# Kernel optimization log

Hardware: AMD Instinct MI355X
Metric: run time of the kernel (lower is better)

## Reference

```python
import jax, jax.numpy as jnp
import numpy as np

INPUT_SIZE = 256
NUM_LABELS = 50
L = NUM_LABELS + 1  # internal label count incl. pad label (index L-1)
B, T = 64, 256


def setup_inputs() -> dict:
    key = jax.random.key(0)
    k = jax.random.split(key, 8)
    inp = {
        "input": jax.random.normal(k[0], (B, T, INPUT_SIZE), dtype=jnp.float32),
        "mask": jnp.ones((B, T), dtype=jnp.float32),
        "target": jax.random.randint(k[1], (B, T), 0, NUM_LABELS),
        # state_nn: Linear(input_size, L)
        "state_W": jax.random.normal(k[2], (INPUT_SIZE, L), dtype=jnp.float32) * 0.05,
        "state_b": jnp.zeros((L,), dtype=jnp.float32),
        # trans_nn: Linear(input_size, L*L) (bigram=True)
        "trans_W": jax.random.normal(k[3], (INPUT_SIZE, L * L), dtype=jnp.float32) * 0.05,
        "trans_b": jnp.zeros((L * L,), dtype=jnp.float32),
    }
    return inp


def _energy(x, mask, state_W, state_b, trans_W, trans_b):
    # out_s: [B,T,L]  (unary scores), out_t: [B,T,L,L] (bigram transitions)
    out_s = jnp.einsum("bti,il->btl", x, state_W) + state_b
    out_t = (jnp.einsum("bti,io->bto", x, trans_W) + trans_b).reshape(
        x.shape[0], x.shape[1], L, L
    )
    energy = out_t + out_s[:, :, None, :]  # [B,T,L,L]
    return energy * mask[:, :, None, None]


def reference(input, mask, target, state_W, state_b, trans_W, trans_b):
    """ChainCRF.loss: -log p(target | input) per batch element, shape [B]."""
    energy = _energy(input, mask, state_W, state_b, trans_W, trans_b)
    e_t = jnp.transpose(energy, (1, 0, 2, 3))  # [T,B,L,L]
    tgt_t = target.T                            # [T,B]
    msk_t = mask.T                              # [T,B]
    bidx = jnp.arange(input.shape[0])

    # t = 0: start from pad label (index L-1)
    partition0 = e_t[0][:, L - 1, :]                       # [B,L]
    tgt0 = e_t[0][bidx, L - 1, tgt_t[0]]                   # [B]

    def step(carry, xs):
        part, tgt_e, prev = carry
        curr, tgt, m = xs  # curr [B,L,L], tgt [B], m [B]
        part_new = jax.nn.logsumexp(curr + part[:, :, None], axis=1)
        part = part + (part_new - part) * m[:, None]
        tgt_e = tgt_e + curr[bidx, prev, tgt]
        return (part, tgt_e, tgt), None

    (part, tgt_e, _), _ = jax.lax.scan(
        step, (partition0, tgt0, tgt_t[0]), (e_t[1:], tgt_t[1:], msk_t[1:])
    )
    return jax.nn.logsumexp(part, axis=1) - tgt_e
```

## Files before the change

### kernel.cpp

```cpp
#include <hip/hip_runtime.h>
#include <hip/hip_bf16.h>

#define B_    64
#define T_    256
#define K_    256
#define L_    51
#define LL_   2601
#define RS_   64
#define NG_   3328
#define PST_  4096
#define MT_   128
#define NT_   128

typedef __bf16 bf16x8 __attribute__((ext_vector_type(8)));
typedef float  f32x4  __attribute__((ext_vector_type(4)));
typedef unsigned int u32x4 __attribute__((ext_vector_type(4)));
typedef u32x4 __attribute__((may_alias)) u32x4_a;

static __device__ __forceinline__ bf16x8 as_bf16x8(u32x4 u) {
    return __builtin_bit_cast(bf16x8, u);
}
static __device__ __forceinline__ unsigned short bf16bits(float x) {
    return __builtin_bit_cast(unsigned short, __float2bfloat16(x));
}
static __device__ __forceinline__ void gld_lds16(const void* g, void* l) {
    __builtin_amdgcn_global_load_lds(
        (const __attribute__((address_space(1))) unsigned int*)g,
        (__attribute__((address_space(3))) unsigned int*)l, 16, 0, 0);
}

#define DPP_STEP(v, OP, CTRL)                                                   \
    {                                                                           \
        int _x = __builtin_bit_cast(int, v);                                    \
        float _o = __builtin_bit_cast(                                          \
            float, __builtin_amdgcn_update_dpp(_x, _x, CTRL, 0xF, 0xF, true));  \
        v = OP(v, _o);                                                          \
    }
static __device__ __forceinline__ float addf(float a, float b) { return a + b; }

__global__ __launch_bounds__(256) void prep_w(
    const float* __restrict__ trans_W, const float* __restrict__ trans_b,
    const float* __restrict__ state_W, const float* __restrict__ state_b,
    __hip_bfloat16* __restrict__ Wt, float* __restrict__ bias)
{
    const int n  = blockIdx.x * 64 + (threadIdx.x >> 2);
    const int kq = (threadIdx.x & 3) * 64;
    const int j  = n >> 6;
    const int i  = n & 63;
    const bool valid = (i < L_) && (j < L_);
    const int o = i * L_ + j;

    __hip_bfloat16 tmp[64];
#pragma unroll
    for (int kk = 0; kk < 64; ++kk) {
        const int k = kq + kk;
        float w = valid ? (trans_W[(size_t)k * LL_ + o] + state_W[k * L_ + j]) : 0.f;
        tmp[kk] = __float2bfloat16(w);
    }
    u32x4* dst = (u32x4*)(Wt + (size_t)n * K_ + kq);
    const u32x4* src = (const u32x4*)tmp;
#pragma unroll
    for (int q = 0; q < 8; ++q) dst[q] = src[q];

    if ((threadIdx.x & 3) == 0)
        bias[n] = valid ? (trans_b[o] + state_b[j]) : 0.f;
}

__global__ void prep_x(const float4* __restrict__ x4, ushort4* __restrict__ xb4, int n4)
{
    for (int idx = blockIdx.x * blockDim.x + threadIdx.x; idx < n4;
         idx += gridDim.x * blockDim.x) {
        float4 v = x4[idx];
        ushort4 o;
        o.x = bf16bits(v.x); o.y = bf16bits(v.y);
        o.z = bf16bits(v.z); o.w = bf16bits(v.w);
        xb4[idx] = o;
    }
}

__global__ void zero_pad(u32x4* __restrict__ P16, int nBT)
{
    const int per = (PST_ - NG_) / 8;
    const int tot = nBT * per;
    const u32x4 z = {};
    for (int idx = blockIdx.x * blockDim.x + threadIdx.x; idx < tot;
         idx += gridDim.x * blockDim.x) {
        const int m = idx / per;
        const int q = idx - m * per;
        P16[(size_t)m * (PST_ / 8) + (NG_ / 8) + q] = z;
    }
}

__global__ __launch_bounds__(256) void gemm_energy(
    const __hip_bfloat16* __restrict__ xb,
    const __hip_bfloat16* __restrict__ Wt,
    const float* __restrict__ bias,
    const float* __restrict__ mask,
    __hip_bfloat16* __restrict__ P,
    int t0, int Tc, int TcShift)
{
    __shared__ __align__(16) __hip_bfloat16 As[MT_ * 128];
    __shared__ __align__(16) __hip_bfloat16 Bs[NT_ * 128];

    const int tid  = threadIdx.x;
    const int lane = tid & 63;
    const int wv   = tid >> 6;
    const int quad = lane >> 4;
    const int l16  = lane & 15;
    const int m0 = blockIdx.y * MT_;
    const int n0 = blockIdx.x * NT_;
    const int mrow0 = (wv >> 1) * 64;
    const int ncol0 = (wv & 1) * 64;

    const int srow = wv * 4 + (lane >> 4);
    const int spos = lane & 15;

    f32x4 acc[4][4] = {};

    for (int kp = 0; kp < 2; ++kp) {
        if (kp) __syncthreads();
#pragma unroll
        for (int it = 0; it < 8; ++it) {
            const int r  = it * 16 + srow;
            const int kc = spos ^ (r & 15);
            const int ma = m0 + r;
            const int rg = (ma >> TcShift) * T_ + t0 + (ma & (Tc - 1));
            gld_lds16((const char*)xb + (size_t)rg * 512 + kp * 256 + kc * 16,
                      (char*)As + it * 4096 + wv * 1024);
            gld_lds16((const char*)Wt + (size_t)(n0 + r) * 512 + kp * 256 + kc * 16,
                      (char*)Bs + it * 4096 + wv * 1024);
        }
        asm volatile("s_waitcnt vmcnt(0)" ::: "memory");
        __syncthreads();

        const u32x4_a* Av = (const u32x4_a*)As;
        const u32x4_a* Bv = (const u32x4_a*)Bs;
#pragma unroll
        for (int kk = 0; kk < 4; ++kk) {
            bf16x8 af[4], bfr[4];
#pragma unroll
            for (int f = 0; f < 4; ++f) {
                const int ra = mrow0 + f * 16 + l16;
                af[f]  = as_bf16x8(Av[ra * 16 + ((kk * 4 + quad) ^ (ra & 15))]);
                const int rb = ncol0 + f * 16 + l16;
                bfr[f] = as_bf16x8(Bv[rb * 16 + ((kk * 4 + quad) ^ (rb & 15))]);
            }
#pragma unroll
            for (int mf = 0; mf < 4; ++mf)
#pragma unroll
                for (int nf = 0; nf < 4; ++nf)
                    acc[mf][nf] = __builtin_amdgcn_mfma_f32_16x16x32_bf16(
                        af[mf], bfr[nf], acc[mf][nf], 0, 0, 0);
        }
    }

    float bv[4]; bool val[4]; int ncol[4], ic[4], jc[4];
#pragma unroll
    for (int nf = 0; nf < 4; ++nf) {
        const int n = n0 + ncol0 + nf * 16 + l16;
        ncol[nf] = n;
        ic[nf] = n & 63;
        jc[nf] = n >> 6;
        val[nf] = (ic[nf] < L_) && (jc[nf] < L_);
        bv[nf]  = bias[n];
    }
#pragma unroll
    for (int mf = 0; mf < 4; ++mf) {
#pragma unroll
        for (int r = 0; r < 4; ++r) {
            const int mloc = m0 + mrow0 + mf * 16 + quad * 4 + r;
            const int bb = mloc >> TcShift;
            const int tl = mloc & (Tc - 1);
            const int t  = t0 + tl;
            const float mval = mask[bb * T_ + t];
            const bool idmask = (mval == 0.f) && (t != 0);
            __hip_bfloat16* prow = P + (size_t)mloc * PST_;
#pragma unroll
            for (int nf = 0; nf < 4; ++nf) {
                float v;
                if (idmask)
                    v = (val[nf] && ic[nf] == jc[nf]) ? 1.f : 0.f;
                else
                    v = val[nf] ? __expf((acc[mf][nf][r] + bv[nf]) * mval) : 0.f;
                prow[ncol[nf]] = __float2bfloat16(v);
            }
        }
    }
}

__global__ __launch_bounds__(256) void prod_quad(
    const __hip_bfloat16* __restrict__ P,
    __hip_bfloat16* __restrict__ Q,
    int Tc)
{
    __shared__ u32x4 Sm[3][512];
    __shared__ __align__(16) unsigned short GL[64 * 72];
    __shared__ __align__(16) unsigned short VT[2][64 * 72];

    const int tid  = threadIdx.x;
    const int wv   = tid >> 6;
    const int lane = tid & 63;
    const int quad = lane >> 4;
    const int l16  = lane & 15;
    const int bq = blockIdx.x;
    const int Tq = Tc >> 2;
    const int b  = bq / Tq;
    const int tq = bq - b * Tq;
    const __hip_bfloat16* tile0 = P + (size_t)(b * Tc + tq * 4) * PST_;

    for (int q = 0; q < 6; ++q) {
        const int idx  = q * 4 + wv;
        const int tile = idx >> 3;
        const int part = idx & 7;
        const int slot = part * 64 + lane;
        const int r    = slot >> 3;
        const int csrc = (slot & 7) ^ (r & 7);
        gld_lds16((const char*)(tile0 + (size_t)(tile + 1) * PST_) + (r * 8 + csrc) * 16,
                  (char*)&Sm[tile][part * 64]);
    }
    const u32x4* g1 = (const u32x4*)tile0;
    u32x4 c0 = g1[tid], c1 = g1[256 + tid];
    asm volatile("s_waitcnt vmcnt(0)" ::: "memory");
    {
        const unsigned short* e0 = (const unsigned short*)&c0;
        const unsigned short* e1 = (const unsigned short*)&c1;
        int j = tid >> 3, i0 = (tid & 7) * 8;
#pragma unroll
        for (int e = 0; e < 8; ++e) GL[(i0 + e) * 72 + j] = e0[e];
        j = (256 + tid) >> 3; i0 = (tid & 7) * 8;
#pragma unroll
        for (int e = 0; e < 8; ++e) GL[(i0 + e) * 72 + j] = e1[e];
    }
    __syncthreads();

    __hip_bfloat16* qout = Q + (size_t)bq * PST_;
    const int ra = wv * 16 + l16;

#pragma unroll
    for (int st = 0; st < 3; ++st) {
        const u32x4* Sa = Sm[st];
        const unsigned short* Bbuf = (st == 0) ? GL : VT[st - 1];
        bf16x8 a[2], bb[4][2];
#pragma unroll
        for (int ks = 0; ks < 2; ++ks)
            a[ks] = as_bf16x8(Sa[ra * 8 + ((ks * 4 + quad) ^ (ra & 7))]);
#pragma unroll
        for (int nf = 0; nf < 4; ++nf) {
            const u32x4_a* brow = (const u32x4_a*)(Bbuf + (nf * 16 + l16) * 72);
#pragma unroll
            for (int ks = 0; ks < 2; ++ks) bb[nf][ks] = as_bf16x8(brow[ks * 4 + quad]);
        }
        f32x4 acc[4] = {};
#pragma unroll
        for (int nf = 0; nf < 4; ++nf) {
            acc[nf] = __builtin_amdgcn_mfma_f32_16x16x32_bf16(a[0], bb[nf][0], acc[nf], 0, 0, 0);
            acc[nf] = __builtin_amdgcn_mfma_f32_16x16x32_bf16(a[1], bb[nf][1], acc[nf], 0, 0, 0);
        }
        if (st < 2) {
#pragma unroll
            for (int nf = 0; nf < 4; ++nf) {
                const int n  = nf * 16 + l16;
                const int mm = wv * 16 + quad * 4;
#pragma unroll
                for (int pr = 0; pr < 2; ++pr) {
                    unsigned int pk = (unsigned int)bf16bits(acc[nf][pr * 2]) |
                                      ((unsigned int)bf16bits(acc[nf][pr * 2 + 1]) << 16);
                    *(unsigned int*)(&VT[st][n * 72 + mm + pr * 2]) = pk;
                }
            }
            __syncthreads();
        } else {
#pragma unroll
            for (int nf = 0; nf < 4; ++nf) {
                const int n = nf * 16 + l16;
#pragma unroll
                for (int r = 0; r < 4; ++r)
                    qout[(wv * 16 + quad * 4 + r) * RS_ + n] = __float2bfloat16(acc[nf][r]);
            }
        }
    }
}

__global__ __launch_bounds__(64) void tgt_kernel(
    const __hip_bfloat16* __restrict__ P, const int* __restrict__ target,
    const float* __restrict__ mask, float* __restrict__ tgt_ws, int t0, int Tc)
{
    const int b = blockIdx.x, lane = threadIdx.x;
    float s = 0.f;
    for (int tl = lane; tl < Tc; tl += 64) {
        const int t = t0 + tl;
        const int j = target[b * T_ + t];
        const int i = (t == 0) ? (L_ - 1) : target[b * T_ + t - 1];
        const float m = (t == 0) ? 1.f : mask[b * T_ + t];
        if (m != 0.f) {
            const float pval = __bfloat162float(P[(size_t)(b * Tc + tl) * PST_ + j * RS_ + i]);
            s += __logf(pval);
        }
    }
#pragma unroll
    for (int d = 1; d < 64; d <<= 1) s += __shfl_xor(s, d);
    if (lane == 0) {
        if (t0 == 0) tgt_ws[b] = s;
        else         tgt_ws[b] += s;
    }
}

__global__ __launch_bounds__(64, 1) void scan_q(
    const __hip_bfloat16* __restrict__ Q,
    float* __restrict__ p_ws, float* __restrict__ ls_ws,
    const float* __restrict__ tgt_ws, float* __restrict__ out,
    int t0q, int Tq, int Tqtot)
{
    __shared__ __align__(16) unsigned short p_arr[64];

    const int b    = blockIdx.x;
    const int lane = threadIdx.x;
    const int quad = lane >> 4;
    const int l16  = lane & 15;

    float pv[4] = {0.f, 0.f, 0.f, 0.f};
    float logscale = 0.f;
    if (t0q == 0) {
        p_arr[lane] = (lane == L_ - 1) ? (unsigned short)0x3F80 : (unsigned short)0;
    } else {
#pragma unroll
        for (int f = 0; f < 4; ++f) pv[f] = p_ws[b * 64 + f * 16 + l16];
        logscale = ls_ws[b];
        p_arr[quad * 16 + l16] = bf16bits(pv[quad]);
    }
    asm volatile("s_waitcnt lgkmcnt(0)" ::: "memory");

    int off[8];
#pragma unroll
    for (int f = 0; f < 4; ++f)
#pragma unroll
        for (int ks = 0; ks < 2; ++ks)
            off[f * 2 + ks] = (f * 16 + l16) * 8 + ks * 4 + quad;

    const u32x4* gp = (const u32x4*)Q + (size_t)b * Tq * (PST_ / 8);
    const u32x4_a* pa = (const u32x4_a*)p_arr;

    u32x4 s0[8], s1[8], s2[8], s3[8];
    auto fetch = [&](u32x4 (&st)[8], int tl) {
        const u32x4* g = gp + (size_t)tl * (PST_ / 8);
#pragma unroll
        for (int q = 0; q < 8; ++q) st[q] = g[off[q]];
    };
    fetch(s0, 0);
    if (1 < Tq) fetch(s1, 1);
    if (2 < Tq) fetch(s2, 2);
    if (3 < Tq) fetch(s3, 3);

    auto step = [&](u32x4 (&st)[8], int tl) {
        bf16x8 a0 = as_bf16x8(pa[quad]);
        bf16x8 a1 = as_bf16x8(pa[4 + quad]);
        const f32x4 z = {};
        f32x4 ae[4], ao[4];
#pragma unroll
        for (int f = 0; f < 4; ++f) {
            ae[f] = __builtin_amdgcn_mfma_f32_16x16x32_bf16(a0, as_bf16x8(st[f * 2 + 0]), z, 0, 0, 0);
            ao[f] = __builtin_amdgcn_mfma_f32_16x16x32_bf16(a1, as_bf16x8(st[f * 2 + 1]), z, 0, 0, 0);
        }
#pragma unroll
        for (int f = 0; f < 4; ++f) pv[f] = ae[f][0] + ao[f][0];

        if (((tl & 1) == 1) || (tl == Tq - 1)) {
            float mx = fmaxf(fmaxf(pv[0], pv[1]), fmaxf(pv[2], pv[3]));
            DPP_STEP(mx, fmaxf, 0xB1);
            DPP_STEP(mx, fmaxf, 0x4E);
            DPP_STEP(mx, fmaxf, 0x124);
            DPP_STEP(mx, fmaxf, 0x128);
            const float inv = 1.f / mx;
            logscale += __logf(mx);
#pragma unroll
            for (int f = 0; f < 4; ++f) pv[f] *= inv;
        }
        p_arr[quad * 16 + l16] = bf16bits(pv[quad]);
        asm volatile("s_waitcnt lgkmcnt(0)" ::: "memory");
    };

    for (int tl = 0; tl < Tq; tl += 4) {
        step(s0, tl);
        if (tl + 4 < Tq) fetch(s0, tl + 4);
        if (tl + 1 < Tq) { step(s1, tl + 1); if (tl + 5 < Tq) fetch(s1, tl + 5); }
        if (tl + 2 < Tq) { step(s2, tl + 2); if (tl + 6 < Tq) fetch(s2, tl + 6); }
        if (tl + 3 < Tq) { step(s3, tl + 3); if (tl + 7 < Tq) fetch(s3, tl + 7); }
    }

    if (t0q + Tq == Tqtot) {
        float s = pv[0] + pv[1] + pv[2] + pv[3];
        DPP_STEP(s, addf, 0xB1);
        DPP_STEP(s, addf, 0x4E);
        DPP_STEP(s, addf, 0x124);
        DPP_STEP(s, addf, 0x128);
        if (lane == 0) out[b] = logscale + __logf(s) - tgt_ws[b];
    } else {
        if (quad == 0) {
#pragma unroll
            for (int f = 0; f < 4; ++f) p_ws[b * 64 + f * 16 + l16] = pv[f];
        }
        if (lane == 0) ls_ws[b] = logscale;
    }
}

extern "C" void kernel_launch(void* const* d_in, const int* in_sizes, int n_in,
                              void* d_out, int out_size, void* d_ws, size_t ws_size,
                              hipStream_t stream)
{
    (void)in_sizes; (void)n_in; (void)out_size;
    const float* x       = (const float*)d_in[0];
    const float* mask    = (const float*)d_in[1];
    const int*   target  = (const int*)d_in[2];
    const float* state_W = (const float*)d_in[3];
    const float* state_b = (const float*)d_in[4];
    const float* trans_W = (const float*)d_in[5];
    const float* trans_b = (const float*)d_in[6];
    float* out = (float*)d_out;

    char* ws = (char*)d_ws;
    size_t off = 0;
    auto alloc = [&](size_t bytes) -> void* {
        void* p = ws + off;
        off = (off + bytes + 255) & ~(size_t)255;
        return p;
    };

    __hip_bfloat16* Wt   = (__hip_bfloat16*)alloc((size_t)NG_ * K_ * 2);
    float*          bias = (float*)alloc((size_t)NG_ * 4);
    __hip_bfloat16* xb   = (__hip_bfloat16*)alloc((size_t)B_ * T_ * K_ * 2);
    float*          p_ws = (float*)alloc((size_t)B_ * 64 * 4);
    float*          ls   = (float*)alloc((size_t)B_ * 4);
    float*          tgte = (float*)alloc((size_t)B_ * 4);
    const size_t fixed = off;

    int Tc = 256;
    while (Tc > 4 && fixed + (size_t)Tc * B_ * PST_ * 2 * 5 / 4 + 512 > ws_size) Tc >>= 1;
    __hip_bfloat16* P = (__hip_bfloat16*)alloc((size_t)Tc * B_ * PST_ * 2);
    __hip_bfloat16* Q = (__hip_bfloat16*)alloc((size_t)(Tc / 4) * B_ * PST_ * 2);
    int TcShift = 0;
    while ((1 << TcShift) < Tc) ++TcShift;

    prep_w<<<dim3(NG_ / 64), 256, 0, stream>>>(trans_W, trans_b, state_W, state_b, Wt, bias);
    prep_x<<<dim3(2048), 256, 0, stream>>>((const float4*)x, (ushort4*)xb, B_ * T_ * K_ / 4);
    zero_pad<<<dim3(2048), 256, 0, stream>>>((u32x4*)P, B_ * Tc);

    for (int t0 = 0; t0 < T_; t0 += Tc) {
        gemm_energy<<<dim3(NG_ / NT_, (B_ * Tc) / MT_), 256, 0, stream>>>(
            xb, Wt, bias, mask, P, t0, Tc, TcShift);
        prod_quad<<<dim3(B_ * (Tc / 4)), 256, 0, stream>>>(P, Q, Tc);
        tgt_kernel<<<dim3(B_), 64, 0, stream>>>(P, target, mask, tgte, t0, Tc);
        scan_q<<<dim3(B_), 64, 0, stream>>>(Q, p_ws, ls, tgte, out,
                                            t0 / 4, Tc / 4, T_ / 4);
    }
}
```

Measured before the change: 230.4 us.

## Tree-reduce four-matrix products and vectorize transposed GEMM epilogue stores

The GEMM epilogue swaps the MFMA operand order so each lane holds four consecutive output columns. It then packs four bf16 values into one 64-bit store and loads the bias as a vector, replacing scalar 2-byte scattered stores. The quad product kernel replaces the serial chain of three dependent matmuls with a tree: two pairwise products run in parallel, then a final product, so the chain is shorter. Transposes are done through MFMA against an identity fragment instead of scalar LDS scatter, and the output is written with coalesced 16-byte stores. The cost is more LDS use and an extra MFMA stage for the transposes.

```diff
diff --git a/kernel.cpp b/kernel.cpp
--- a/kernel.cpp
+++ b/kernel.cpp
@@ -11,17 +11,24 @@
 #define PST_  4096
 #define MT_   128
 #define NT_   128
+#define TS_   72
 
 typedef __bf16 bf16x8 __attribute__((ext_vector_type(8)));
 typedef float  f32x4  __attribute__((ext_vector_type(4)));
 typedef unsigned int u32x4 __attribute__((ext_vector_type(4)));
 typedef u32x4 __attribute__((may_alias)) u32x4_a;
+typedef unsigned long long ull;
+typedef ull __attribute__((may_alias)) ull_a;
 
 static __device__ __forceinline__ bf16x8 as_bf16x8(u32x4 u) {
     return __builtin_bit_cast(bf16x8, u);
 }
 static __device__ __forceinline__ unsigned short bf16bits(float x) {
     return __builtin_bit_cast(unsigned short, __float2bfloat16(x));
+}
+static __device__ __forceinline__ ull pack4(f32x4 a) {
+    return (ull)bf16bits(a[0]) | ((ull)bf16bits(a[1]) << 16) |
+           ((ull)bf16bits(a[2]) << 32) | ((ull)bf16bits(a[3]) << 48);
 }
 static __device__ __forceinline__ void gld_lds16(const void* g, void* l) {
     __builtin_amdgcn_global_load_lds(
@@ -146,44 +153,41 @@
                 bfr[f] = as_bf16x8(Bv[rb * 16 + ((kk * 4 + quad) ^ (rb & 15))]);
             }
 #pragma unroll
-            for (int mf = 0; mf < 4; ++mf)
-#pragma unroll
-                for (int nf = 0; nf < 4; ++nf)
-                    acc[mf][nf] = __builtin_amdgcn_mfma_f32_16x16x32_bf16(
-                        af[mf], bfr[nf], acc[mf][nf], 0, 0, 0);
-        }
-    }
-
-    float bv[4]; bool val[4]; int ncol[4], ic[4], jc[4];
-#pragma unroll
-    for (int nf = 0; nf < 4; ++nf) {
-        const int n = n0 + ncol0 + nf * 16 + l16;
-        ncol[nf] = n;
-        ic[nf] = n & 63;
-        jc[nf] = n >> 6;
-        val[nf] = (ic[nf] < L_) && (jc[nf] < L_);
-        bv[nf]  = bias[n];
-    }
+            for (int nf = 0; nf < 4; ++nf)
+#pragma unroll
+                for (int mf = 0; mf < 4; ++mf)
+                    acc[nf][mf] = __builtin_amdgcn_mfma_f32_16x16x32_bf16(
+                        bfr[nf], af[mf], acc[nf][mf], 0, 0, 0);
+        }
+    }
+
+    const int jcol = (n0 + ncol0) >> 6;
+    const bool jok = jcol < L_;
 #pragma unroll
     for (int mf = 0; mf < 4; ++mf) {
-#pragma unroll
-        for (int r = 0; r < 4; ++r) {
-            const int mloc = m0 + mrow0 + mf * 16 + quad * 4 + r;
-            const int bb = mloc >> TcShift;
-            const int tl = mloc & (Tc - 1);
-            const int t  = t0 + tl;
-            const float mval = mask[bb * T_ + t];
-            const bool idmask = (mval == 0.f) && (t != 0);
-            __hip_bfloat16* prow = P + (size_t)mloc * PST_;
-#pragma unroll
-            for (int nf = 0; nf < 4; ++nf) {
+        const int m  = m0 + mrow0 + mf * 16 + l16;
+        const int bb = m >> TcShift;
+        const int tl = m & (Tc - 1);
+        const int t  = t0 + tl;
+        const float mval = mask[bb * T_ + t];
+        const bool idm = (mval == 0.f) && (t != 0);
+        __hip_bfloat16* prow = P + (size_t)m * PST_;
+#pragma unroll
+        for (int nf = 0; nf < 4; ++nf) {
+            const int nbase = n0 + ncol0 + nf * 16 + quad * 4;
+            const int ibase = nf * 16 + quad * 4;
+            const f32x4 bv = *(const f32x4*)(bias + nbase);
+            ull pk = 0;
+#pragma unroll
+            for (int r = 0; r < 4; ++r) {
+                const int i = ibase + r;
+                const bool ok = jok && (i < L_);
                 float v;
-                if (idmask)
-                    v = (val[nf] && ic[nf] == jc[nf]) ? 1.f : 0.f;
-                else
-                    v = val[nf] ? __expf((acc[mf][nf][r] + bv[nf]) * mval) : 0.f;
-                prow[ncol[nf]] = __float2bfloat16(v);
+                if (idm) v = (ok && i == jcol) ? 1.f : 0.f;
+                else     v = ok ? __expf((acc[nf][mf][r] + bv[r]) * mval) : 0.f;
+                pk |= (ull)bf16bits(v) << (16 * r);
             }
+            *(ull_a*)(prow + nbase) = pk;
         }
     }
 }
@@ -193,9 +197,11 @@
     __hip_bfloat16* __restrict__ Q,
     int Tc)
 {
-    __shared__ u32x4 Sm[3][512];
-    __shared__ __align__(16) unsigned short GL[64 * 72];
-    __shared__ __align__(16) unsigned short VT[2][64 * 72];
+    __shared__ u32x4 Sm[4][512];
+    __shared__ __align__(16) unsigned short T1t[64 * TS_];
+    __shared__ __align__(16) unsigned short T3t[64 * TS_];
+    __shared__ __align__(16) unsigned short W2t[64 * TS_];
+    __shared__ __align__(16) unsigned short W4b[64 * TS_];
 
     const int tid  = threadIdx.x;
     const int wv   = tid >> 6;
@@ -208,76 +214,99 @@
     const int tq = bq - b * Tq;
     const __hip_bfloat16* tile0 = P + (size_t)(b * Tc + tq * 4) * PST_;
 
-    for (int q = 0; q < 6; ++q) {
+#pragma unroll
+    for (int q = 0; q < 8; ++q) {
         const int idx  = q * 4 + wv;
         const int tile = idx >> 3;
         const int part = idx & 7;
         const int slot = part * 64 + lane;
         const int r    = slot >> 3;
         const int csrc = (slot & 7) ^ (r & 7);
-        gld_lds16((const char*)(tile0 + (size_t)(tile + 1) * PST_) + (r * 8 + csrc) * 16,
+        gld_lds16((const char*)(tile0 + (size_t)tile * PST_) + (r * 8 + csrc) * 16,
                   (char*)&Sm[tile][part * 64]);
     }
-    const u32x4* g1 = (const u32x4*)tile0;
-    u32x4 c0 = g1[tid], c1 = g1[256 + tid];
+
+    u32x4 idf[2];
+    {
+        const int e = l16 & 7;
+        const unsigned int bits = (e & 1) ? 0x3F800000u : 0x3F80u;
+#pragma unroll
+        for (int par = 0; par < 2; ++par) {
+            u32x4 v = {};
+            if (quad == (l16 >> 3) + par * 2) v[e >> 1] = bits;
+            idf[par] = v;
+        }
+    }
+
+    const int ra = wv * 16 + l16;
+    const f32x4 z = {};
     asm volatile("s_waitcnt vmcnt(0)" ::: "memory");
+    __syncthreads();
+
+#pragma unroll
+    for (int tt = 0; tt < 2; ++tt) {
+        const u32x4* S = Sm[tt * 2];
+        bf16x8 a0 = as_bf16x8(S[ra * 8 + (quad ^ (ra & 7))]);
+        bf16x8 a1 = as_bf16x8(S[ra * 8 + ((4 + quad) ^ (ra & 7))]);
+        unsigned short* dst = tt ? T3t : T1t;
+#pragma unroll
+        for (int nf = 0; nf < 4; ++nf) {
+            f32x4 d = __builtin_amdgcn_mfma_f32_16x16x32_bf16(
+                (nf >> 1) ? a1 : a0, as_bf16x8(idf[nf & 1]), z, 0, 0, 0);
+            *(ull_a*)(dst + (nf * 16 + l16) * TS_ + wv * 16 + quad * 4) = pack4(d);
+        }
+    }
+    __syncthreads();
+
     {
-        const unsigned short* e0 = (const unsigned short*)&c0;
-        const unsigned short* e1 = (const unsigned short*)&c1;
-        int j = tid >> 3, i0 = (tid & 7) * 8;
-#pragma unroll
-        for (int e = 0; e < 8; ++e) GL[(i0 + e) * 72 + j] = e0[e];
-        j = (256 + tid) >> 3; i0 = (tid & 7) * 8;
-#pragma unroll
-        for (int e = 0; e < 8; ++e) GL[(i0 + e) * 72 + j] = e1[e];
+        bf16x8 a2[2], a3[2];
+#pragma unroll
+        for (int ks = 0; ks < 2; ++ks) {
+            a2[ks] = as_bf16x8(Sm[1][ra * 8 + ((ks * 4 + quad) ^ (ra & 7))]);
+            a3[ks] = as_bf16x8(*(const u32x4_a*)(T3t + ra * TS_ + ks * 32 + quad * 8));
+        }
+#pragma unroll
+        for (int nf = 0; nf < 4; ++nf) {
+            const int rb = nf * 16 + l16;
+            f32x4 u = z, v = z;
+#pragma unroll
+            for (int ks = 0; ks < 2; ++ks) {
+                bf16x8 bU = as_bf16x8(*(const u32x4_a*)(T1t + rb * TS_ + ks * 32 + quad * 8));
+                bf16x8 bV = as_bf16x8(Sm[3][rb * 8 + ((ks * 4 + quad) ^ (rb & 7))]);
+                u = __builtin_amdgcn_mfma_f32_16x16x32_bf16(a2[ks], bU, u, 0, 0, 0);
+                v = __builtin_amdgcn_mfma_f32_16x16x32_bf16(a3[ks], bV, v, 0, 0, 0);
+            }
+            *(ull_a*)(W2t + rb * TS_ + wv * 16 + quad * 4) = pack4(u);
+            *(ull_a*)(W4b + rb * TS_ + wv * 16 + quad * 4) = pack4(v);
+        }
     }
     __syncthreads();
 
-    __hip_bfloat16* qout = Q + (size_t)bq * PST_;
-    const int ra = wv * 16 + l16;
-
-#pragma unroll
-    for (int st = 0; st < 3; ++st) {
-        const u32x4* Sa = Sm[st];
-        const unsigned short* Bbuf = (st == 0) ? GL : VT[st - 1];
-        bf16x8 a[2], bb[4][2];
+    {
+        bf16x8 aw[2];
 #pragma unroll
         for (int ks = 0; ks < 2; ++ks)
-            a[ks] = as_bf16x8(Sa[ra * 8 + ((ks * 4 + quad) ^ (ra & 7))]);
+            aw[ks] = as_bf16x8(*(const u32x4_a*)(W2t + ra * TS_ + ks * 32 + quad * 8));
 #pragma unroll
         for (int nf = 0; nf < 4; ++nf) {
-            const u32x4_a* brow = (const u32x4_a*)(Bbuf + (nf * 16 + l16) * 72);
-#pragma unroll
-            for (int ks = 0; ks < 2; ++ks) bb[nf][ks] = as_bf16x8(brow[ks * 4 + quad]);
-        }
-        f32x4 acc[4] = {};
-#pragma unroll
-        for (int nf = 0; nf < 4; ++nf) {
-            acc[nf] = __builtin_amdgcn_mfma_f32_16x16x32_bf16(a[0], bb[nf][0], acc[nf], 0, 0, 0);
-            acc[nf] = __builtin_amdgcn_mfma_f32_16x16x32_bf16(a[1], bb[nf][1], acc[nf], 0, 0, 0);
-        }
-        if (st < 2) {
-#pragma unroll
-            for (int nf = 0; nf < 4; ++nf) {
-                const int n  = nf * 16 + l16;
-                const int mm = wv * 16 + quad * 4;
-#pragma unroll
-                for (int pr = 0; pr < 2; ++pr) {
-                    unsigned int pk = (unsigned int)bf16bits(acc[nf][pr * 2]) |
-                                      ((unsigned int)bf16bits(acc[nf][pr * 2 + 1]) << 16);
-                    *(unsigned int*)(&VT[st][n * 72 + mm + pr * 2]) = pk;
-                }
+            const int rb = nf * 16 + l16;
+            f32x4 d = z;
+#pragma unroll
+            for (int ks = 0; ks < 2; ++ks) {
+                bf16x8 bw = as_bf16x8(*(const u32x4_a*)(W4b + rb * TS_ + ks * 32 + quad * 8));
+                d = __builtin_amdgcn_mfma_f32_16x16x32_bf16(aw[ks], bw, d, 0, 0, 0);
             }
-            __syncthreads();
-        } else {
-#pragma unroll
-            for (int nf = 0; nf < 4; ++nf) {
-                const int n = nf * 16 + l16;
-#pragma unroll
-                for (int r = 0; r < 4; ++r)
-                    qout[(wv * 16 + quad * 4 + r) * RS_ + n] = __float2bfloat16(acc[nf][r]);
-            }
-        }
+            *(ull_a*)(T1t + rb * TS_ + wv * 16 + quad * 4) = pack4(d);
+        }
+    }
+    __syncthreads();
+
+    u32x4* qout = (u32x4*)(Q + (size_t)bq * PST_);
+#pragma unroll
+    for (int c = tid; c < 512; c += 256) {
+        const int row = c >> 3;
+        const int pos = c & 7;
+        qout[row * 8 + pos] = *(const u32x4_a*)(T1t + row * TS_ + pos * 8);
     }
 }
 
```

After: 229.8 us. Within noise of the previous version (-0.2%).
